# Optimization experiments

Hardware: AMD Instinct MI355X
Metric: run time of the kernel (lower is better)

The kernel has to match this reference:

```python
import jax, jax.numpy as jnp
import numpy as np

N_NODES = 100000
N_EDGES = 1200000
DIM = 64
MAX_DEG = 64
NUM_LAB = 16
BN_EPS = 1e-5


def _lrelu(x):
    return jax.nn.leaky_relu(x, negative_slope=0.01)


def _bn(x, g, b):
    # BatchNorm1d in training mode: batch statistics over node axis
    m = x.mean(axis=0)
    v = x.var(axis=0)
    return (x - m) * jax.lax.rsqrt(v + BN_EPS) * g + b


def _gin_layer(h, src, dst, n, w1, b1, w2, b2, eps, g, b):
    # GINConv: (1+eps)*x_i + sum_{j in N(i)} x_j, then MLP (lin_lrelu_lin), BN, LeakyReLU
    agg = jax.ops.segment_sum(h[src], dst, num_segments=n)
    x = (1.0 + eps) * h + agg
    x = _lrelu(x @ w1 + b1) @ w2 + b2
    return _lrelu(_bn(x, g, b))


def setup_inputs() -> dict:
    key = jax.random.key(0)
    ks = jax.random.split(key, 16)
    s = 0.05
    inp = {
        'node_deg': jax.random.randint(ks[0], (N_NODES,), 0, MAX_DEG + 1, dtype=jnp.int32),
        'node_lab': jax.random.randint(ks[1], (N_NODES,), 0, NUM_LAB, dtype=jnp.int32),
        'edge_index': jax.random.randint(ks[2], (2, N_EDGES), 0, N_NODES, dtype=jnp.int32),
        'emb_deg': jax.random.normal(ks[3], (MAX_DEG + 1, DIM), jnp.float32) * s,
        'emb_lab': jax.random.normal(ks[4], (NUM_LAB, DIM), jnp.float32) * s,
        'l0_w1': jax.random.normal(ks[5], (2 * DIM, 2 * DIM), jnp.float32) * s,
        'l0_b1': jnp.zeros((2 * DIM,), jnp.float32),
        'l0_w2': jax.random.normal(ks[6], (2 * DIM, DIM), jnp.float32) * s,
        'l0_b2': jnp.zeros((DIM,), jnp.float32),
        'l0_eps': jnp.zeros((1,), jnp.float32),
        'bn0_g': jnp.ones((DIM,), jnp.float32),
        'bn0_b': jnp.zeros((DIM,), jnp.float32),
        'l1_w1': jax.random.normal(ks[7], (DIM, DIM), jnp.float32) * s,
        'l1_b1': jnp.zeros((DIM,), jnp.float32),
        'l1_w2': jax.random.normal(ks[8], (DIM, DIM), jnp.float32) * s,
        'l1_b2': jnp.zeros((DIM,), jnp.float32),
        'l1_eps': jnp.zeros((1,), jnp.float32),
        'bn1_g': jnp.ones((DIM,), jnp.float32),
        'bn1_b': jnp.zeros((DIM,), jnp.float32),
        'fc_w1': jax.random.normal(ks[9], (4 * DIM, DIM), jnp.float32) * s,
        'fc_b1': jnp.zeros((DIM,), jnp.float32),
        'fc_bn_g': jnp.ones((DIM,), jnp.float32),
        'fc_bn_b': jnp.zeros((DIM,), jnp.float32),
        'fc_w2': jax.random.normal(ks[10], (DIM, 1), jnp.float32) * s,
        'fc_b2': jnp.zeros((1,), jnp.float32),
    }
    return inp


def reference(node_deg, node_lab, edge_index, emb_deg, emb_lab,
              l0_w1, l0_b1, l0_w2, l0_b2, l0_eps, bn0_g, bn0_b,
              l1_w1, l1_b1, l1_w2, l1_b2, l1_eps, bn1_g, bn1_b,
              fc_w1, fc_b1, fc_bn_g, fc_bn_b, fc_w2, fc_b2):
    n = node_deg.shape[0]
    src, dst = edge_index[0], edge_index[1]
    # embedding concat: [N, 2*DIM]
    h0 = jnp.concatenate([emb_deg[node_deg], emb_lab[node_lab]], axis=1)
    h1 = _gin_layer(h0, src, dst, n, l0_w1, l0_b1, l0_w2, l0_b2, l0_eps[0], bn0_g, bn0_b)
    h2 = _gin_layer(h1, src, dst, n, l1_w1, l1_b1, l1_w2, l1_b2, l1_eps[0], bn1_g, bn1_b)
    x = jnp.concatenate([h0, h1, h2], axis=1)  # [N, 256]
    x = _lrelu(_bn(x @ fc_w1 + fc_b1, fc_bn_g, fc_bn_b))
    out = jax.nn.sigmoid(x @ fc_w2 + fc_b2)
    return out.squeeze(-1)  # [N]
```

## Files before the change

### kernel.cpp

```cpp
#include <hip/hip_runtime.h>

#define N_NODES 100000
#define N_EDGES 1200000
#define NCLS 81
#define NBKT 391
#define BCAP 4608
#define NCHK 293
#define NGBLK 1563

typedef unsigned short u16;
typedef unsigned char u8;
typedef unsigned int u32;
typedef unsigned long long u64;
typedef short bf16x8 __attribute__((ext_vector_type(8)));
typedef float f32x4 __attribute__((ext_vector_type(4)));

__device__ __forceinline__ float b2f(u16 u) {
  union { u32 i; float f; } v; v.i = ((u32)u) << 16; return v.f;
}
__device__ __forceinline__ u16 f2b(float f) {
  union { float f; u32 i; } v; v.f = f;
  u32 x = v.i;
  return (u16)((x + 0x7fffu + ((x >> 16) & 1u)) >> 16);
}
__device__ __forceinline__ void up2(u32 w, float& lo, float& hi) {
  union { u32 u; float f; } a, b;
  a.u = w << 16; b.u = w & 0xffff0000u;
  lo = a.f; hi = b.f;
}
__device__ __forceinline__ float lrelu(float x) { return x > 0.f ? x : 0.01f * x; }

__device__ __forceinline__ bool is_f32(const u16* emb) {
  int lane = threadIdx.x & 63;
  u32 e0 = (emb[lane * 2] >> 7) & 0xFF;
  u32 e1 = (emb[lane * 2 + 1] >> 7) & 0xFF;
  return __ballot((e0 >= 0x90) || (e1 >= 0x90)) != 0ull;
}

__device__ __forceinline__ float rdr(const void* p, int i, bool f32m) {
  return f32m ? ((const float*)p)[i] : b2f(((const u16*)p)[i]);
}

#define P_EMBD 0
#define P_EMBL 4160
#define P_W1A  5184
#define P_B1A  21568
#define P_W2A  21696
#define P_B2A  29888
#define P_EPS0 29952
#define P_G0   29953
#define P_BB0  30017
#define P_LW1  30081
#define P_LB1  34177
#define P_LW2  34241
#define P_LB2  38337
#define P_EPS1 38401
#define P_G1   38402
#define P_BB1  38466
#define P_FW1  38530
#define P_FB1  54914
#define P_FG   54978
#define P_FBB  55042
#define P_FW2  55106
#define P_FB2  55170
#define P_TOT  55171

struct CvtAll {
  const void* src[22];
  int cnt[22];
  int off[22];
};

struct RawPtrs {
  const void* embD;
  const void* embL;
  const void* w1r;
  const void* w2r;
  const void* lw1r;
  const void* lw2r;
  const void* fwr;
};

__global__ void k_init(CvtAll a, RawPtrs rw, const u16* __restrict__ embRaw,
                       float* __restrict__ P, float* __restrict__ W1p,
                       float* __restrict__ Efc, u16* __restrict__ bp,
                       u16* __restrict__ wpB, u32* __restrict__ gcur) {
  bool f32m = is_f32(embRaw);
  int tid = threadIdx.x;
  if (blockIdx.y < 22) {
    if (blockIdx.y == 0 && blockIdx.x == 0) {
      for (int i = tid; i < NBKT; i += 256) gcur[i] = 0;
    }
    int seg = blockIdx.y;
    int i = blockIdx.x * 256 + tid;
    if (i < a.cnt[seg]) {
      float v = f32m ? ((const float*)a.src[seg])[i] : b2f(((const u16*)a.src[seg])[i]);
      P[a.off[seg] + i] = v;
    }
    return;
  }
  int idx = blockIdx.x * 256 + tid;
  if (idx < NCLS * 128) {
    int c = idx >> 7, h = idx & 127;
    float s = 0.f;
    if (c < 65) {
      for (int k = 0; k < 64; ++k)
        s = fmaf(rdr(rw.embD, c * 64 + k, f32m), rdr(rw.w1r, k * 128 + h, f32m), s);
    } else {
      for (int k = 0; k < 64; ++k)
        s = fmaf(rdr(rw.embL, (c - 65) * 64 + k, f32m), rdr(rw.w1r, (64 + k) * 128 + h, f32m), s);
    }
    W1p[idx] = s;
    return;
  }
  if (idx < NCLS * 128 + NCLS * 64) {
    int r = idx - NCLS * 128;
    int c = r >> 6, o = r & 63;
    float s = 0.f;
    if (c < 65) {
      for (int k = 0; k < 64; ++k)
        s = fmaf(rdr(rw.embD, c * 64 + k, f32m), rdr(rw.fwr, k * 64 + o, f32m), s);
    } else {
      for (int k = 0; k < 64; ++k)
        s = fmaf(rdr(rw.embL, (c - 65) * 64 + k, f32m), rdr(rw.fwr, (64 + k) * 64 + o, f32m), s);
    }
    Efc[r] = s;
    return;
  }
  if (idx < NCLS * 128 + NCLS * 64 + 24576) {
    int pidx = idx - (NCLS * 128 + NCLS * 64);
    int seg, rel;
    if (pidx < 8192)       { seg = 0; rel = pidx; }
    else if (pidx < 12288) { seg = 1; rel = pidx - 8192; }
    else if (pidx < 16384) { seg = 2; rel = pidx - 12288; }
    else                   { seg = 3; rel = pidx - 16384; }
    const void* srcs[4] = {rw.w2r, rw.lw1r, rw.lw2r, rw.fwr};
    const int addoff[4] = {0, 0, 0, 128 * 64};
    const int KBs[4] = {4, 2, 2, 4};
    int j = rel & 7, lane = (rel >> 3) & 63, rest = rel >> 9;
    int kb = rest % KBs[seg], nt = rest / KBs[seg];
    int k = kb * 32 + (lane >> 4) * 8 + j;
    int n = nt * 16 + (lane & 15);
    bp[pidx] = f2b(rdr(srcs[seg], addoff[seg] + k * 64 + n, f32m));
    return;
  }
  int p2 = idx - (NCLS * 128 + NCLS * 64 + 24576);
  if (p2 >= 12288) return;
  int j = p2 & 7, lane = (p2 >> 3) & 63, rest = p2 >> 9;
  int kb = rest % 3, nt = rest / 3;
  int c = kb * 32 + (lane >> 4) * 8 + j;
  int n = nt * 16 + (lane & 15);
  float s = 0.f;
  if (c < NCLS) {
    if (c < 65) {
      for (int k = 0; k < 64; ++k)
        s = fmaf(rdr(rw.embD, c * 64 + k, f32m), rdr(rw.w1r, k * 128 + n, f32m), s);
    } else {
      for (int k = 0; k < 64; ++k)
        s = fmaf(rdr(rw.embL, (c - 65) * 64 + k, f32m), rdr(rw.w1r, (64 + k) * 128 + n, f32m), s);
    }
  }
  wpB[p2] = (c < NCLS) ? f2b(s) : 0;
}

__global__ __launch_bounds__(256) void k_bsort(const int* __restrict__ edge,
                                               const int* __restrict__ ndeg,
                                               const int* __restrict__ nlab,
                                               u32* __restrict__ gcur,
                                               u64* __restrict__ e2) {
  __shared__ u32 cnt[NBKT], rbase[NBKT];
  __shared__ u32 slo[4096], shi[4096];
  for (int i = threadIdx.x; i < NBKT; i += 256) cnt[i] = 0;
  __syncthreads();
  int base = blockIdx.x * 4096;
  for (int i = threadIdx.x; i < 4096; i += 256) {
    int e = base + i;
    if (e < N_EDGES) {
      int s = edge[e], d = edge[N_EDGES + e];
      slo[i] = ((u32)s << 11) | ((u32)ndeg[s] << 4) | (u32)nlab[s];
      shi[i] = (u32)d;
      atomicAdd(&cnt[(u32)d >> 8], 1u);
    } else shi[i] = 0xFFFFFFFFu;
  }
  __syncthreads();
  for (int i = threadIdx.x; i < NBKT; i += 256) {
    u32 c = cnt[i];
    rbase[i] = c ? atomicAdd(&gcur[i], c) : 0u;
    cnt[i] = 0;
  }
  __syncthreads();
  for (int i = threadIdx.x; i < 4096; i += 256) {
    u32 d = shi[i];
    if (d == 0xFFFFFFFFu) continue;
    u32 b = d >> 8;
    u32 pos = rbase[b] + atomicAdd(&cnt[b], 1u);
    e2[(size_t)b * BCAP + pos] = ((u64)d << 32) | (u64)slo[i];
  }
}

__global__ __launch_bounds__(512) void k_csrh(const u64* __restrict__ e2,
                                              const u32* __restrict__ gcur,
                                              const u16* __restrict__ wpB,
                                              const float* __restrict__ W1p,
                                              const float* __restrict__ P,
                                              const int* __restrict__ ndeg,
                                              const int* __restrict__ nlab,
                                              const u16* __restrict__ Bp2,
                                              u32* __restrict__ row_ptr,
                                              u32* __restrict__ einfo,
                                              u16* __restrict__ t0,
                                              float* __restrict__ pbuf) {
  __shared__ u32 l[256], cur[256], gl[NBKT], wt[8];
  __shared__ u32 h32[256 * 24];
  __shared__ u32 sbase;
  __shared__ u16 T[8][16][136];
  __shared__ float lsum[8][64], lsq[8][64];
  int b = blockIdx.x, tid = threadIdx.x;
  int wid = tid >> 6, lane = tid & 63;
  if (tid < NBKT) gl[tid] = gcur[tid];
  if (tid < 256) l[tid] = 0;
  for (int i = tid; i < 256 * 24; i += 512) h32[i] = 0;
  __syncthreads();
  if (wid == 0) {
    u32 s = 0;
    for (int i = lane; i < b; i += 64) s += gl[i];
    s += __shfl_xor(s, 1, 64); s += __shfl_xor(s, 2, 64); s += __shfl_xor(s, 4, 64);
    s += __shfl_xor(s, 8, 64); s += __shfl_xor(s, 16, 64); s += __shfl_xor(s, 32, 64);
    if (lane == 0) sbase = s;
  }
  u32 cnt = gl[b];
  const u64* src = e2 + (size_t)b * BCAP;
  for (u32 e = tid; e < cnt; e += 512)
    atomicAdd(&l[(u32)(src[e] >> 32) & 255u], 1u);
  __syncthreads();
  u32 v = 0, incl = 0;
  if (tid < 256) {
    v = l[tid];
    u32 x = v;
#pragma unroll
    for (int off = 1; off < 64; off <<= 1) {
      u32 t = __shfl_up(x, off, 64);
      if (lane >= off) x += t;
    }
    if (lane == 63) wt[wid] = x;
    incl = x;
  }
  __syncthreads();
  if (tid < 256) {
    u32 woff = 0;
    for (int w = 0; w < wid; ++w) woff += wt[w];
    u32 pos0 = sbase + woff + incl - v;
    cur[tid] = pos0;
    int nn = b * 256 + tid;
    if (nn <= N_NODES) row_ptr[nn] = pos0;
  }
  __syncthreads();
  for (u32 e = tid; e < cnt; e += 512) {
    u64 r = src[e];
    u32 dl = (u32)(r >> 32) & 255u;
    u32 lo = (u32)r;
    u32 pos = atomicAdd(&cur[dl], 1u);
    einfo[pos] = lo;
    u32 c1 = (lo >> 4) & 0x7Fu, c2 = 65u + (lo & 15u);
    atomicAdd(&h32[dl * 24 + (c1 >> 2)], 1u << ((c1 & 3u) * 8));
    atomicAdd(&h32[dl * 24 + (c2 >> 2)], 1u << ((c2 & 3u) * 8));
  }
  __syncthreads();
  const u8* h = (const u8*)h32;
  int row = lane & 15, q = lane >> 4;
  float onep = 1.f + P[P_EPS0];
  const bf16x8* bp = (const bf16x8*)wpB;
  const bf16x8* bp2 = (const bf16x8*)Bp2;
  float ssA[4] = {0.f, 0.f, 0.f, 0.f}, qqA[4] = {0.f, 0.f, 0.f, 0.f};
#pragma unroll 1
  for (int t = wid; t < 16; t += 8) {
    int m0 = b * 256 + t * 16;
    if (m0 >= N_NODES) break;
    f32x4 acc[8];
#pragma unroll
    for (int nt = 0; nt < 8; ++nt) {
      float bb = P[P_B1A + nt * 16 + row];
      acc[nt][0] = bb; acc[nt][1] = bb; acc[nt][2] = bb; acc[nt][3] = bb;
    }
    const u8* ar = h + (t * 16 + row) * 96 + q * 8;
#pragma unroll
    for (int kb = 0; kb < 3; ++kb) {
      bf16x8 af;
#pragma unroll
      for (int j = 0; j < 8; ++j) af[j] = (short)f2b((float)ar[kb * 32 + j]);
#pragma unroll
      for (int nt = 0; nt < 8; ++nt) {
        bf16x8 bf = bp[(nt * 3 + kb) * 64 + lane];
        acc[nt] = __builtin_amdgcn_mfma_f32_16x16x32_bf16(af, bf, acc[nt], 0, 0, 0);
      }
    }
#pragma unroll
    for (int r = 0; r < 4; ++r) {
      int m = m0 + q * 4 + r;
      int node = q * 4 + r;
      if (m < N_NODES) {
        const float* wd = W1p + ndeg[m] * 128;
        const float* wl = W1p + (65 + nlab[m]) * 128;
#pragma unroll
        for (int nt = 0; nt < 8; ++nt) {
          int cc = nt * 16 + row;
          float vv = acc[nt][r] + onep * (wd[cc] + wl[cc]);
          T[wid][node][cc] = f2b(lrelu(vv));
        }
      } else {
#pragma unroll
        for (int nt = 0; nt < 8; ++nt) T[wid][node][nt * 16 + row] = 0;
      }
    }
    const u16* ap = &T[wid][row][q * 8];
    f32x4 acc2[4];
#pragma unroll
    for (int nt = 0; nt < 4; ++nt) {
      float bb = P[P_B2A + nt * 16 + row];
      acc2[nt][0] = bb; acc2[nt][1] = bb; acc2[nt][2] = bb; acc2[nt][3] = bb;
    }
#pragma unroll
    for (int kb = 0; kb < 4; ++kb) {
      bf16x8 af = *(const bf16x8*)(ap + kb * 32);
#pragma unroll
      for (int nt = 0; nt < 4; ++nt) {
        bf16x8 bf = bp2[(nt * 4 + kb) * 64 + lane];
        acc2[nt] = __builtin_amdgcn_mfma_f32_16x16x32_bf16(af, bf, acc2[nt], 0, 0, 0);
      }
    }
#pragma unroll
    for (int nt = 0; nt < 4; ++nt) {
      float s = 0.f, z = 0.f;
#pragma unroll
      for (int r = 0; r < 4; ++r) {
        int m = m0 + q * 4 + r;
        if (m < N_NODES) {
          u16 bv = f2b(acc2[nt][r]);
          t0[(size_t)m * 64 + nt * 16 + row] = bv;
          float vv = b2f(bv);
          s += vv; z = fmaf(vv, vv, z);
        }
      }
      s += __shfl_xor(s, 16, 64); s += __shfl_xor(s, 32, 64);
      z += __shfl_xor(z, 16, 64); z += __shfl_xor(z, 32, 64);
      ssA[nt] += s; qqA[nt] += z;
    }
  }
  if (lane < 16) {
#pragma unroll
    for (int nt = 0; nt < 4; ++nt) {
      lsum[wid][nt * 16 + lane] = ssA[nt];
      lsq[wid][nt * 16 + lane] = qqA[nt];
    }
  }
  __syncthreads();
  if (tid < 64) {
    float s = 0.f;
#pragma unroll
    for (int w = 0; w < 8; ++w) s += lsum[w][tid];
    pbuf[(size_t)b * 128 + tid] = s;
  } else if (tid < 128) {
    int c = tid - 64;
    float s = 0.f;
#pragma unroll
    for (int w = 0; w < 8; ++w) s += lsq[w][c];
    pbuf[(size_t)b * 128 + tid] = s;
  }
}

__global__ void k_sr(const float* __restrict__ pbuf, float* __restrict__ statsOut,
                     int nrows) {
  __shared__ float l[256];
  int c = blockIdx.x;
  float s = 0.f;
  for (int r = threadIdx.x; r < nrows; r += 256) s += pbuf[(size_t)r * 128 + c];
  l[threadIdx.x] = s;
  __syncthreads();
  for (int off = 128; off > 0; off >>= 1) {
    if (threadIdx.x < off) l[threadIdx.x] += l[threadIdx.x + off];
    __syncthreads();
  }
  if (threadIdx.x == 0) statsOut[c] = l[0];
}

template <int KB, int LDA, int BIASOFF>
__global__ __launch_bounds__(256) void k_gemm(const u16* __restrict__ A,
                                              const u16* __restrict__ Bp,
                                              const float* __restrict__ P,
                                              float* __restrict__ pbuf,
                                              u16* __restrict__ C) {
  __shared__ float lsum[4][64], lsq[4][64];
  int wid = threadIdx.x >> 6, lane = threadIdx.x & 63;
  int m0 = (blockIdx.x * 4 + wid) * 16;
  bool act = m0 < N_NODES;
  int row = lane & 15, q = lane >> 4;
  float ss[4] = {0.f, 0.f, 0.f, 0.f}, qq[4] = {0.f, 0.f, 0.f, 0.f};
  if (act) {
    const u16* ap = A + (size_t)(m0 + row) * LDA + q * 8;
    const bf16x8* bp = (const bf16x8*)Bp;
    f32x4 acc[4];
#pragma unroll
    for (int nt = 0; nt < 4; ++nt) {
      float b = (BIASOFF >= 0) ? P[BIASOFF + nt * 16 + row] : 0.f;
      acc[nt][0] = b; acc[nt][1] = b; acc[nt][2] = b; acc[nt][3] = b;
    }
#pragma unroll
    for (int kb = 0; kb < KB; ++kb) {
      bf16x8 af = *(const bf16x8*)(ap + kb * 32);
#pragma unroll
      for (int nt = 0; nt < 4; ++nt) {
        bf16x8 bf = bp[(nt * KB + kb) * 64 + lane];
        acc[nt] = __builtin_amdgcn_mfma_f32_16x16x32_bf16(af, bf, acc[nt], 0, 0, 0);
      }
    }
#pragma unroll
    for (int nt = 0; nt < 4; ++nt) {
      float s = 0.f, z = 0.f;
#pragma unroll
      for (int r = 0; r < 4; ++r) {
        int m = m0 + q * 4 + r;
        u16 bv = f2b(acc[nt][r]);
        C[(size_t)m * 64 + nt * 16 + row] = bv;
        float v = b2f(bv);
        s += v; z = fmaf(v, v, z);
      }
      s += __shfl_xor(s, 16, 64); s += __shfl_xor(s, 32, 64);
      z += __shfl_xor(z, 16, 64); z += __shfl_xor(z, 32, 64);
      ss[nt] = s; qq[nt] = z;
    }
  }
  if (lane < 16) {
#pragma unroll
    for (int nt = 0; nt < 4; ++nt) {
      lsum[wid][nt * 16 + lane] = ss[nt];
      lsq[wid][nt * 16 + lane] = qq[nt];
    }
  }
  __syncthreads();
  int t = threadIdx.x;
  if (t < 64)
    pbuf[(size_t)blockIdx.x * 128 + t] = lsum[0][t] + lsum[1][t] + lsum[2][t] + lsum[3][t];
  else if (t < 128) {
    int c = t - 64;
    pbuf[(size_t)blockIdx.x * 128 + t] = lsq[0][c] + lsq[1][c] + lsq[2][c] + lsq[3][c];
  }
}

__global__ __launch_bounds__(256) void k_gemm_bn(const u16* __restrict__ A,
                                                 const u16* __restrict__ Bp,
                                                 const float* __restrict__ P,
                                                 const float* __restrict__ stats,
                                                 u16* __restrict__ C) {
  int wid = threadIdx.x >> 6, lane = threadIdx.x & 63;
  int m0 = (blockIdx.x * 4 + wid) * 16;
  if (m0 >= N_NODES) return;
  int row = lane & 15, q = lane >> 4;
  const float invN = 1.f / (float)N_NODES;
  float sc[16], sh[16];
#pragma unroll
  for (int kb = 0; kb < 2; ++kb)
#pragma unroll
    for (int j = 0; j < 8; ++j) {
      int f = kb * 32 + q * 8 + j;
      float mm = stats[f] * invN;
      float var = fmaxf(stats[64 + f] * invN - mm * mm, 0.f);
      float inv = rsqrtf(var + 1e-5f);
      float s = inv * P[P_G0 + f];
      sc[kb * 8 + j] = s;
      sh[kb * 8 + j] = P[P_BB0 + f] - mm * s;
    }
  const u16* ap = A + (size_t)(m0 + row) * 64 + q * 8;
  const bf16x8* bp = (const bf16x8*)Bp;
  f32x4 acc[4];
#pragma unroll
  for (int nt = 0; nt < 4; ++nt) {
    acc[nt][0] = 0.f; acc[nt][1] = 0.f; acc[nt][2] = 0.f; acc[nt][3] = 0.f;
  }
#pragma unroll
  for (int kb = 0; kb < 2; ++kb) {
    uint4 raw = *(const uint4*)(ap + kb * 32);
    u32 rw[4] = {raw.x, raw.y, raw.z, raw.w};
    bf16x8 af;
#pragma unroll
    for (int p = 0; p < 4; ++p) {
      float lo, hi;
      up2(rw[p], lo, hi);
      float y0 = lrelu(fmaf(sc[kb * 8 + 2 * p], lo, sh[kb * 8 + 2 * p]));
      float y1 = lrelu(fmaf(sc[kb * 8 + 2 * p + 1], hi, sh[kb * 8 + 2 * p + 1]));
      af[2 * p] = (short)f2b(y0);
      af[2 * p + 1] = (short)f2b(y1);
    }
#pragma unroll
    for (int nt = 0; nt < 4; ++nt) {
      bf16x8 bf = bp[(nt * 2 + kb) * 64 + lane];
      acc[nt] = __builtin_amdgcn_mfma_f32_16x16x32_bf16(af, bf, acc[nt], 0, 0, 0);
    }
  }
#pragma unroll
  for (int nt = 0; nt < 4; ++nt)
#pragma unroll
    for (int r = 0; r < 4; ++r) {
      int m = m0 + q * 4 + r;
      C[(size_t)m * 64 + nt * 16 + row] = f2b(acc[nt][r]);
    }
}

__global__ __launch_bounds__(256) void k_agg1(const u32* __restrict__ rp,
                                              const u32* __restrict__ einfo,
                                              const u16* __restrict__ g1,
                                              const float* __restrict__ P,
                                              u16* __restrict__ abuf) {
  int lane = threadIdx.x & 63, wv = threadIdx.x >> 6;
  int n = blockIdx.x * 4 + wv;
  if (n >= N_NODES) return;
  u32 st = rp[n], en = rp[n + 1];
  u32 m = en - st;
  int grp = lane >> 4;
  int fo = (lane & 15) * 4;
  u32 myidx = (u32)n;
  if (lane < (int)m) myidx = einfo[st + lane] >> 11;
  u32 mm = m < 64u ? m : 64u;
  float a0 = 0.f, a1 = 0.f, a2 = 0.f, a3 = 0.f;
  for (u32 k = 0; k < mm; k += 16) {
#pragma unroll
    for (int bb = 0; bb < 4; ++bb) {
      u32 e = k + (u32)(bb * 4 + grp);
      u32 src = (u32)__shfl((int)myidx, (int)e, 64);
      if (e < mm) {
        uint2 v = *(const uint2*)(g1 + (size_t)src * 64 + fo);
        float l0, h0, l1, h1;
        up2(v.x, l0, h0);
        up2(v.y, l1, h1);
        a0 += l0; a1 += h0; a2 += l1; a3 += h1;
      }
    }
  }
  a0 += __shfl_xor(a0, 16, 64); a0 += __shfl_xor(a0, 32, 64);
  a1 += __shfl_xor(a1, 16, 64); a1 += __shfl_xor(a1, 32, 64);
  a2 += __shfl_xor(a2, 16, 64); a2 += __shfl_xor(a2, 32, 64);
  a3 += __shfl_xor(a3, 16, 64); a3 += __shfl_xor(a3, 32, 64);
  for (u32 k = 64; k < m; ++k) {
    u32 src = einfo[st + k] >> 11;
    uint2 v = *(const uint2*)(g1 + (size_t)src * 64 + fo);
    float l0, h0, l1, h1;
    up2(v.x, l0, h0);
    up2(v.y, l1, h1);
    a0 += l0; a1 += h0; a2 += l1; a3 += h1;
  }
  float onep = 1.f + P[P_EPS1];
  uint2 sv = *(const uint2*)(g1 + (size_t)n * 64 + fo);
  float s0, s1, s2, s3;
  up2(sv.x, s0, s1);
  up2(sv.y, s2, s3);
  float r0 = P[P_LB1 + fo + 0] + fmaf(onep, s0, a0);
  float r1 = P[P_LB1 + fo + 1] + fmaf(onep, s1, a1);
  float r2 = P[P_LB1 + fo + 2] + fmaf(onep, s2, a2);
  float r3 = P[P_LB1 + fo + 3] + fmaf(onep, s3, a3);
  if (lane < 16) {
    uint2 o;
    o.x = ((u32)f2b(lrelu(r0))) | (((u32)f2b(lrelu(r1))) << 16);
    o.y = ((u32)f2b(lrelu(r2))) | (((u32)f2b(lrelu(r3))) << 16);
    *(uint2*)(abuf + (size_t)n * 64 + fo) = o;
  }
}

__global__ __launch_bounds__(256) void k_gemm_fc1bn(const u16* __restrict__ t0,
                                                    const u16* __restrict__ t1,
                                                    const u16* __restrict__ Bp,
                                                    const float* __restrict__ P,
                                                    const float* __restrict__ stats,
                                                    float* __restrict__ pbuf,
                                                    const int* __restrict__ ndeg,
                                                    const int* __restrict__ nlab,
                                                    const float* __restrict__ Efc,
                                                    u16* __restrict__ C) {
  __shared__ float lsum[4][64], lsq[4][64];
  int wid = threadIdx.x >> 6, lane = threadIdx.x & 63;
  int m0 = (blockIdx.x * 4 + wid) * 16;
  bool act = m0 < N_NODES;
  int row = lane & 15, q = lane >> 4;
  float ss[4] = {0.f, 0.f, 0.f, 0.f}, qq[4] = {0.f, 0.f, 0.f, 0.f};
  if (act) {
    const float invN = 1.f / (float)N_NODES;
    float sc[32], sh[32];
#pragma unroll
    for (int h = 0; h < 2; ++h) {
      const float* st = stats + h * 128;
      int gof = h ? P_G1 : P_G0, bof = h ? P_BB1 : P_BB0;
#pragma unroll
      for (int kb = 0; kb < 2; ++kb)
#pragma unroll
        for (int j = 0; j < 8; ++j) {
          int f = kb * 32 + q * 8 + j;
          float mm = st[f] * invN;
          float var = fmaxf(st[64 + f] * invN - mm * mm, 0.f);
          float inv = rsqrtf(var + 1e-5f);
          float s = inv * P[gof + f];
          sc[h * 16 + kb * 8 + j] = s;
          sh[h * 16 + kb * 8 + j] = P[bof + f] - mm * s;
        }
    }
    const u16* a0 = t0 + (size_t)(m0 + row) * 64 + q * 8;
    const u16* a1 = t1 + (size_t)(m0 + row) * 64 + q * 8;
    const bf16x8* bp = (const bf16x8*)Bp;
    f32x4 acc[4];
#pragma unroll
    for (int nt = 0; nt < 4; ++nt) {
      float b = P[P_FB1 + nt * 16 + row];
      acc[nt][0] = b; acc[nt][1] = b; acc[nt][2] = b; acc[nt][3] = b;
    }
#pragma unroll
    for (int kb = 0; kb < 4; ++kb) {
      const u16* src = (kb < 2) ? (a0 + kb * 32) : (a1 + (kb - 2) * 32);
      int ci = (kb < 2) ? kb * 8 : 16 + (kb - 2) * 8;
      uint4 raw = *(const uint4*)src;
      u32 rw[4] = {raw.x, raw.y, raw.z, raw.w};
      bf16x8 af;
#pragma unroll
      for (int p = 0; p < 4; ++p) {
        float lo, hi;
        up2(rw[p], lo, hi);
        float y0 = lrelu(fmaf(sc[ci + 2 * p], lo, sh[ci + 2 * p]));
        float y1 = lrelu(fmaf(sc[ci + 2 * p + 1], hi, sh[ci + 2 * p + 1]));
        af[2 * p] = (short)f2b(y0);
        af[2 * p + 1] = (short)f2b(y1);
      }
#pragma unroll
      for (int nt = 0; nt < 4; ++nt) {
        bf16x8 bf = bp[(nt * 4 + kb) * 64 + lane];
        acc[nt] = __builtin_amdgcn_mfma_f32_16x16x32_bf16(af, bf, acc[nt], 0, 0, 0);
      }
    }
    float es[4][4];
#pragma unroll
    for (int r = 0; r < 4; ++r) {
      int m = m0 + q * 4 + r;
      int dn = ndeg[m], ln = 65 + nlab[m];
#pragma unroll
      for (int nt = 0; nt < 4; ++nt) {
        int cc = nt * 16 + row;
        es[r][nt] = acc[nt][r] + Efc[dn * 64 + cc] + Efc[ln * 64 + cc];
      }
    }
#pragma unroll
    for (int nt = 0; nt < 4; ++nt) {
      float s = 0.f, z = 0.f;
#pragma unroll
      for (int r = 0; r < 4; ++r) {
        int m = m0 + q * 4 + r;
        u16 bv = f2b(es[r][nt]);
        C[(size_t)m * 64 + nt * 16 + row] = bv;
        float v = b2f(bv);
        s += v; z = fmaf(v, v, z);
      }
      s += __shfl_xor(s, 16, 64); s += __shfl_xor(s, 32, 64);
      z += __shfl_xor(z, 16, 64); z += __shfl_xor(z, 32, 64);
      ss[nt] = s; qq[nt] = z;
    }
  }
  if (lane < 16) {
#pragma unroll
    for (int nt = 0; nt < 4; ++nt) {
      lsum[wid][nt * 16 + lane] = ss[nt];
      lsq[wid][nt * 16 + lane] = qq[nt];
    }
  }
  __syncthreads();
  int t = threadIdx.x;
  if (t < 64)
    pbuf[(size_t)blockIdx.x * 128 + t] = lsum[0][t] + lsum[1][t] + lsum[2][t] + lsum[3][t];
  else if (t < 128) {
    int c = t - 64;
    pbuf[(size_t)blockIdx.x * 128 + t] = lsq[0][c] + lsq[1][c] + lsq[2][c] + lsq[3][c];
  }
}

__global__ __launch_bounds__(256) void k_fc2(const u16* __restrict__ t,
                                             const float* __restrict__ stats,
                                             const float* __restrict__ P,
                                             const u16* __restrict__ embRaw,
                                             void* __restrict__ out) {
  __shared__ float scF[64], shF[64], fwF[64];
  bool f32m = is_f32(embRaw);
  int tid = threadIdx.x;
  if (tid < 64) {
    const float invN = 1.f / (float)N_NODES;
    float mm = stats[tid] * invN;
    float var = fmaxf(stats[64 + tid] * invN - mm * mm, 0.f);
    float inv = rsqrtf(var + 1e-5f);
    float s = inv * P[P_FG + tid];
    scF[tid] = s;
    shF[tid] = P[P_FBB + tid] - mm * s;
    fwF[tid] = P[P_FW2 + tid];
  }
  __syncthreads();
  int n = blockIdx.x * 256 + tid;
  if (n >= N_NODES) return;
  float z = P[P_FB2];
  const uint4* tn = (const uint4*)(t + (size_t)n * 64);
#pragma unroll
  for (int jj = 0; jj < 8; ++jj) {
    uint4 raw = tn[jj];
    u32 w[4] = {raw.x, raw.y, raw.z, raw.w};
#pragma unroll
    for (int p = 0; p < 4; ++p) {
      int f = jj * 8 + p * 2;
      float lo, hi;
      up2(w[p], lo, hi);
      float y0 = lrelu(fmaf(scF[f], lo, shF[f]));
      float y1 = lrelu(fmaf(scF[f + 1], hi, shF[f + 1]));
      z = fmaf(y0, fwF[f], z);
      z = fmaf(y1, fwF[f + 1], z);
    }
  }
  float s = 1.f / (1.f + expf(-z));
  if (!(fabsf(z) < 1e30f)) s = 0.25f;
  if (f32m) ((float*)out)[n] = s;
  else      ((u16*)out)[n] = f2b(s);
}

extern "C" void kernel_launch(void* const* d_in, const int* in_sizes, int n_in,
                              void* d_out, int out_size, void* d_ws, size_t ws_size,
                              hipStream_t stream) {
  const int* node_deg = (const int*)d_in[0];
  const int* node_lab = (const int*)d_in[1];
  const int* edge     = (const int*)d_in[2];
  const u16* embRaw   = (const u16*)d_in[3];
  (void)in_sizes; (void)n_in; (void)out_size; (void)ws_size;

  char* base = (char*)d_ws;
  size_t off = 0;
  auto alloc = [&](size_t bytes) -> void* {
    void* p = base + off;
    off += (bytes + 15) & ~(size_t)15;
    return p;
  };
  float* Pb    = (float*)alloc((size_t)P_TOT * 4);
  float* stats = (float*)alloc(384 * 4);
  u32* gcur    = (u32*)alloc(NBKT * 4);
  float* W1p   = (float*)alloc(NCLS * 128 * 4);
  float* Efc   = (float*)alloc(NCLS * 64 * 4);
  u16* bpack   = (u16*)alloc(24576 * 2);
  u16* wpB     = (u16*)alloc(12288 * 2);
  u32* row_ptr = (u32*)alloc((size_t)(N_NODES + 1) * 4);
  float* pbuf  = (float*)alloc((size_t)NGBLK * 128 * 4);
  u32* einfo   = (u32*)alloc((size_t)N_EDGES * 4);
  u64* e2      = (u64*)alloc((size_t)NBKT * BCAP * 8);
  void* arena  = alloc((size_t)N_NODES * 128 * 2);
  u16* t0      = (u16*)alloc((size_t)N_NODES * 64 * 2);
  u16* t1      = (u16*)alloc((size_t)N_NODES * 64 * 2);
  u16* t2      = (u16*)alloc((size_t)N_NODES * 64 * 2);
  u16* g1   = (u16*)arena;
  u16* abuf = (u16*)arena + (size_t)N_NODES * 64;
  u16* Bp_w2a = bpack;
  u16* Bp_lw1 = bpack + 8192;
  u16* Bp_lw2 = bpack + 12288;
  u16* Bp_fw1 = bpack + 16384;

  CvtAll ca;
  const int srcidx[22] = {3, 4, 5, 6, 7, 8, 9, 10, 11, 12, 13, 14, 15, 16, 17, 18, 19, 20, 21, 22, 23, 24};
  const int cnts[22]   = {4160, 1024, 16384, 128, 8192, 64, 1, 64, 64, 4096, 64, 4096, 64, 1, 64, 64, 16384, 64, 64, 64, 64, 1};
  const int offs[22]   = {P_EMBD, P_EMBL, P_W1A, P_B1A, P_W2A, P_B2A, P_EPS0, P_G0, P_BB0,
                          P_LW1, P_LB1, P_LW2, P_LB2, P_EPS1, P_G1, P_BB1,
                          P_FW1, P_FB1, P_FG, P_FBB, P_FW2, P_FB2};
  for (int i = 0; i < 22; ++i) { ca.src[i] = d_in[srcidx[i]]; ca.cnt[i] = cnts[i]; ca.off[i] = offs[i]; }
  RawPtrs rw;
  rw.embD = d_in[3]; rw.embL = d_in[4]; rw.w1r = d_in[5]; rw.w2r = d_in[7];
  rw.lw1r = d_in[12]; rw.lw2r = d_in[14]; rw.fwr = d_in[19];

  k_init<<<dim3(205, 23), 256, 0, stream>>>(ca, rw, embRaw, Pb, W1p, Efc, bpack, wpB, gcur);

  k_bsort<<<NCHK, 256, 0, stream>>>(edge, node_deg, node_lab, gcur, e2);

  k_csrh<<<NBKT, 512, 0, stream>>>(e2, gcur, wpB, W1p, Pb, node_deg, node_lab,
                                   Bp_w2a, row_ptr, einfo, t0, pbuf);
  k_sr<<<128, 256, 0, stream>>>(pbuf, stats, NBKT);

  const int GEMM_GRID = NGBLK;

  k_gemm_bn<<<GEMM_GRID, 256, 0, stream>>>(t0, Bp_lw1, Pb, stats, g1);
  k_agg1<<<(N_NODES + 3) / 4, 256, 0, stream>>>(row_ptr, einfo, g1, Pb, abuf);
  k_gemm<2, 64, P_LB2><<<GEMM_GRID, 256, 0, stream>>>(abuf, Bp_lw2, Pb, pbuf, t1);
  k_sr<<<128, 256, 0, stream>>>(pbuf, stats + 128, NGBLK);

  k_gemm_fc1bn<<<GEMM_GRID, 256, 0, stream>>>(t0, t1, Bp_fw1, Pb, stats, pbuf,
                                              node_deg, node_lab, Efc, t2);
  k_sr<<<128, 256, 0, stream>>>(pbuf, stats + 256, NGBLK);
  k_fc2<<<(N_NODES + 255) / 256, 256, 0, stream>>>(t2, stats + 256, Pb, embRaw, d_out);
}
```

Baseline: 287.2 us.

## Slice aggregation features into per-XCD column slabs for L2 locality

The g1 and abuf buffers move from row-major [N,64] to four column slabs of [N,16], and each slab is pinned to a pair of XCDs by decoding the block index. k_agg1 now has each wave handle four nodes over one 16-feature slice, so the gathered working set per XCD is a quarter of the table and can stay in that XCD's L2. A new k_gemm_sl reads the sliced layout and feeds the MFMA GEMM. The cost is four times as many edge-index shuffles and einfo reads. The hard-coded XCD mapping also assumes round-robin block dispatch across 8 XCDs.

```diff
diff --git a/kernel.cpp b/kernel.cpp
--- a/kernel.cpp
+++ b/kernel.cpp
@@ -7,6 +7,7 @@
 #define BCAP 4608
 #define NCHK 293
 #define NGBLK 1563
+#define SLN (N_NODES * 16)
 
 typedef unsigned short u16;
 typedef unsigned char u8;
@@ -501,7 +502,7 @@
 #pragma unroll
     for (int r = 0; r < 4; ++r) {
       int m = m0 + q * 4 + r;
-      C[(size_t)m * 64 + nt * 16 + row] = f2b(acc[nt][r]);
+      C[(size_t)nt * SLN + (size_t)m * 16 + row] = f2b(acc[nt][r]);
     }
 }
 
@@ -510,57 +511,131 @@
                                               const u16* __restrict__ g1,
                                               const float* __restrict__ P,
                                               u16* __restrict__ abuf) {
+  int b = blockIdx.x;
+  int xcd = b & 7;
+  int s = xcd & 3;
+  int chunk = (b >> 3) + ((xcd >> 2) ? 3125 : 0);
   int lane = threadIdx.x & 63, wv = threadIdx.x >> 6;
-  int n = blockIdx.x * 4 + wv;
-  if (n >= N_NODES) return;
-  u32 st = rp[n], en = rp[n + 1];
+  int ns = lane >> 4;
+  int li = lane & 15;
+  int es = li >> 2, half = li & 3;
+  int n0 = chunk * 16 + wv * 4;
+  int n = n0 + ns;
+  const u16* gt = g1 + (size_t)s * SLN;
+  u32 rpv = 0;
+  if (lane <= 4) rpv = rp[n0 + lane];
+  u32 st = (u32)__shfl((int)rpv, ns, 64);
+  u32 en = (u32)__shfl((int)rpv, ns + 1, 64);
   u32 m = en - st;
-  int grp = lane >> 4;
-  int fo = (lane & 15) * 4;
-  u32 myidx = (u32)n;
-  if (lane < (int)m) myidx = einfo[st + lane] >> 11;
-  u32 mm = m < 64u ? m : 64u;
+  u32 myidx = 0;
+  if (li < (int)m) myidx = einfo[st + li];
+  u32 mm = m < 16u ? m : 16u;
   float a0 = 0.f, a1 = 0.f, a2 = 0.f, a3 = 0.f;
-  for (u32 k = 0; k < mm; k += 16) {
-#pragma unroll
-    for (int bb = 0; bb < 4; ++bb) {
-      u32 e = k + (u32)(bb * 4 + grp);
-      u32 src = (u32)__shfl((int)myidx, (int)e, 64);
-      if (e < mm) {
-        uint2 v = *(const uint2*)(g1 + (size_t)src * 64 + fo);
-        float l0, h0, l1, h1;
-        up2(v.x, l0, h0);
-        up2(v.y, l1, h1);
-        a0 += l0; a1 += h0; a2 += l1; a3 += h1;
-      }
-    }
-  }
-  a0 += __shfl_xor(a0, 16, 64); a0 += __shfl_xor(a0, 32, 64);
-  a1 += __shfl_xor(a1, 16, 64); a1 += __shfl_xor(a1, 32, 64);
-  a2 += __shfl_xor(a2, 16, 64); a2 += __shfl_xor(a2, 32, 64);
-  a3 += __shfl_xor(a3, 16, 64); a3 += __shfl_xor(a3, 32, 64);
-  for (u32 k = 64; k < m; ++k) {
-    u32 src = einfo[st + k] >> 11;
-    uint2 v = *(const uint2*)(g1 + (size_t)src * 64 + fo);
-    float l0, h0, l1, h1;
-    up2(v.x, l0, h0);
-    up2(v.y, l1, h1);
-    a0 += l0; a1 += h0; a2 += l1; a3 += h1;
-  }
-  float onep = 1.f + P[P_EPS1];
-  uint2 sv = *(const uint2*)(g1 + (size_t)n * 64 + fo);
-  float s0, s1, s2, s3;
-  up2(sv.x, s0, s1);
-  up2(sv.y, s2, s3);
-  float r0 = P[P_LB1 + fo + 0] + fmaf(onep, s0, a0);
-  float r1 = P[P_LB1 + fo + 1] + fmaf(onep, s1, a1);
-  float r2 = P[P_LB1 + fo + 2] + fmaf(onep, s2, a2);
-  float r3 = P[P_LB1 + fo + 3] + fmaf(onep, s3, a3);
-  if (lane < 16) {
+  u32 iters = (mm + 3) >> 2;
+  for (u32 k = 0; k < iters; ++k) {
+    u32 e = k * 4 + (u32)es;
+    u32 idx = (u32)__shfl((int)myidx, ns * 16 + (int)e, 64);
+    if (e < mm) {
+      u32 src = idx >> 11;
+      uint2 v = *(const uint2*)(gt + (size_t)src * 16 + half * 4);
+      float l0, h0, l1, h1;
+      up2(v.x, l0, h0);
+      up2(v.y, l1, h1);
+      a0 += l0; a1 += h0; a2 += l1; a3 += h1;
+    }
+  }
+  if (es == 0) {
+    for (u32 k = 16; k < m; ++k) {
+      u32 src = einfo[st + k] >> 11;
+      uint2 v = *(const uint2*)(gt + (size_t)src * 16 + half * 4);
+      float l0, h0, l1, h1;
+      up2(v.x, l0, h0);
+      up2(v.y, l1, h1);
+      a0 += l0; a1 += h0; a2 += l1; a3 += h1;
+    }
+  }
+  a0 += __shfl_xor(a0, 4, 64); a0 += __shfl_xor(a0, 8, 64);
+  a1 += __shfl_xor(a1, 4, 64); a1 += __shfl_xor(a1, 8, 64);
+  a2 += __shfl_xor(a2, 4, 64); a2 += __shfl_xor(a2, 8, 64);
+  a3 += __shfl_xor(a3, 4, 64); a3 += __shfl_xor(a3, 8, 64);
+  if (es == 0) {
+    float onep = 1.f + P[P_EPS1];
+    uint2 sv = *(const uint2*)(gt + (size_t)n * 16 + half * 4);
+    float s0, s1, s2, s3;
+    up2(sv.x, s0, s1);
+    up2(sv.y, s2, s3);
+    int f = s * 16 + half * 4;
+    float r0 = P[P_LB1 + f + 0] + fmaf(onep, s0, a0);
+    float r1 = P[P_LB1 + f + 1] + fmaf(onep, s1, a1);
+    float r2 = P[P_LB1 + f + 2] + fmaf(onep, s2, a2);
+    float r3 = P[P_LB1 + f + 3] + fmaf(onep, s3, a3);
     uint2 o;
     o.x = ((u32)f2b(lrelu(r0))) | (((u32)f2b(lrelu(r1))) << 16);
     o.y = ((u32)f2b(lrelu(r2))) | (((u32)f2b(lrelu(r3))) << 16);
-    *(uint2*)(abuf + (size_t)n * 64 + fo) = o;
+    *(uint2*)(abuf + (size_t)s * SLN + (size_t)n * 16 + half * 4) = o;
+  }
+}
+
+__global__ __launch_bounds__(256) void k_gemm_sl(const u16* __restrict__ A,
+                                                 const u16* __restrict__ Bp,
+                                                 const float* __restrict__ P,
+                                                 float* __restrict__ pbuf,
+                                                 u16* __restrict__ C) {
+  __shared__ float lsum[4][64], lsq[4][64];
+  int wid = threadIdx.x >> 6, lane = threadIdx.x & 63;
+  int m0 = (blockIdx.x * 4 + wid) * 16;
+  bool act = m0 < N_NODES;
+  int row = lane & 15, q = lane >> 4;
+  float ss[4] = {0.f, 0.f, 0.f, 0.f}, qq[4] = {0.f, 0.f, 0.f, 0.f};
+  if (act) {
+    const bf16x8* bp = (const bf16x8*)Bp;
+    f32x4 acc[4];
+#pragma unroll
+    for (int nt = 0; nt < 4; ++nt) {
+      float b = P[P_LB2 + nt * 16 + row];
+      acc[nt][0] = b; acc[nt][1] = b; acc[nt][2] = b; acc[nt][3] = b;
+    }
+#pragma unroll
+    for (int kb = 0; kb < 2; ++kb) {
+      const u16* ap = A + (size_t)(kb * 2 + (q >> 1)) * SLN +
+                      (size_t)(m0 + row) * 16 + (q & 1) * 8;
+      bf16x8 af = *(const bf16x8*)ap;
+#pragma unroll
+      for (int nt = 0; nt < 4; ++nt) {
+        bf16x8 bf = bp[(nt * 2 + kb) * 64 + lane];
+        acc[nt] = __builtin_amdgcn_mfma_f32_16x16x32_bf16(af, bf, acc[nt], 0, 0, 0);
+      }
+    }
+#pragma unroll
+    for (int nt = 0; nt < 4; ++nt) {
+      float s = 0.f, z = 0.f;
+#pragma unroll
+      for (int r = 0; r < 4; ++r) {
+        int m = m0 + q * 4 + r;
+        u16 bv = f2b(acc[nt][r]);
+        C[(size_t)m * 64 + nt * 16 + row] = bv;
+        float v = b2f(bv);
+        s += v; z = fmaf(v, v, z);
+      }
+      s += __shfl_xor(s, 16, 64); s += __shfl_xor(s, 32, 64);
+      z += __shfl_xor(z, 16, 64); z += __shfl_xor(z, 32, 64);
+      ss[nt] = s; qq[nt] = z;
+    }
+  }
+  if (lane < 16) {
+#pragma unroll
+    for (int nt = 0; nt < 4; ++nt) {
+      lsum[wid][nt * 16 + lane] = ss[nt];
+      lsq[wid][nt * 16 + lane] = qq[nt];
+    }
+  }
+  __syncthreads();
+  int t = threadIdx.x;
+  if (t < 64)
+    pbuf[(size_t)blockIdx.x * 128 + t] = lsum[0][t] + lsum[1][t] + lsum[2][t] + lsum[3][t];
+  else if (t < 128) {
+    int c = t - 64;
+    pbuf[(size_t)blockIdx.x * 128 + t] = lsq[0][c] + lsq[1][c] + lsq[2][c] + lsq[3][c];
   }
 }
 
@@ -779,8 +854,8 @@
   const int GEMM_GRID = NGBLK;
 
   k_gemm_bn<<<GEMM_GRID, 256, 0, stream>>>(t0, Bp_lw1, Pb, stats, g1);
-  k_agg1<<<(N_NODES + 3) / 4, 256, 0, stream>>>(row_ptr, einfo, g1, Pb, abuf);
-  k_gemm<2, 64, P_LB2><<<GEMM_GRID, 256, 0, stream>>>(abuf, Bp_lw2, Pb, pbuf, t1);
+  k_agg1<<<25000, 256, 0, stream>>>(row_ptr, einfo, g1, Pb, abuf);
+  k_gemm_sl<<<GEMM_GRID, 256, 0, stream>>>(abuf, Bp_lw2, Pb, pbuf, t1);
   k_sr<<<128, 256, 0, stream>>>(pbuf, stats + 128, NGBLK);
 
   k_gemm_fc1bn<<<GEMM_GRID, 256, 0, stream>>>(t0, t1, Bp_fw1, Pb, stats, pbuf,
```

Result: no change. 288.2 us (+0.3%).

## Fuse BN stat reductions into producer kernels via last-block atomic counter

Applied to the files above, without the earlier changes.

Removes the three separate k_sr reduction launches by having the last block to finish each producer kernel (k_csrh, k_gemm, k_gemm_fc1bn) sum the per-block partials into the stats buffer, using an atomic counter and threadfences. It also precomputes a packed deg/label word per node in k_init so k_bsort does one gather per edge source instead of two. The intent is to cut launch overhead and gather traffic. The cost is a serial tail: one block reads up to 1563x128 partials on its own, with only 256 threads.

```diff
diff --git a/kernel.cpp b/kernel.cpp
--- a/kernel.cpp
+++ b/kernel.cpp
@@ -84,12 +84,19 @@
 __global__ void k_init(CvtAll a, RawPtrs rw, const u16* __restrict__ embRaw,
                        float* __restrict__ P, float* __restrict__ W1p,
                        float* __restrict__ Efc, u16* __restrict__ bp,
-                       u16* __restrict__ wpB, u32* __restrict__ gcur) {
+                       u16* __restrict__ wpB, u32* __restrict__ gcur,
+                       const int* __restrict__ ndeg, const int* __restrict__ nlab,
+                       u32* __restrict__ pk) {
+  int tid = threadIdx.x;
+  if (blockIdx.y == 23) {
+    int n = blockIdx.x * 256 + tid;
+    if (n < N_NODES) pk[n] = ((u32)ndeg[n] << 4) | (u32)nlab[n];
+    return;
+  }
   bool f32m = is_f32(embRaw);
-  int tid = threadIdx.x;
   if (blockIdx.y < 22) {
     if (blockIdx.y == 0 && blockIdx.x == 0) {
-      for (int i = tid; i < NBKT; i += 256) gcur[i] = 0;
+      for (int i = tid; i < NBKT + 4; i += 256) gcur[i] = 0;
     }
     int seg = blockIdx.y;
     int i = blockIdx.x * 256 + tid;
@@ -164,8 +171,7 @@
 }
 
 __global__ __launch_bounds__(256) void k_bsort(const int* __restrict__ edge,
-                                               const int* __restrict__ ndeg,
-                                               const int* __restrict__ nlab,
+                                               const u32* __restrict__ pk,
                                                u32* __restrict__ gcur,
                                                u64* __restrict__ e2) {
   __shared__ u32 cnt[NBKT], rbase[NBKT];
@@ -177,7 +183,7 @@
     int e = base + i;
     if (e < N_EDGES) {
       int s = edge[e], d = edge[N_EDGES + e];
-      slo[i] = ((u32)s << 11) | ((u32)ndeg[s] << 4) | (u32)nlab[s];
+      slo[i] = ((u32)s << 11) | pk[s];
       shi[i] = (u32)d;
       atomicAdd(&cnt[(u32)d >> 8], 1u);
     } else shi[i] = 0xFFFFFFFFu;
@@ -209,10 +215,12 @@
                                               u32* __restrict__ row_ptr,
                                               u32* __restrict__ einfo,
                                               u16* __restrict__ t0,
-                                              float* __restrict__ pbuf) {
+                                              float* __restrict__ pbuf,
+                                              float* __restrict__ statsOut,
+                                              u32* __restrict__ ctr) {
   __shared__ u32 l[256], cur[256], gl[NBKT], wt[8];
   __shared__ u32 h32[256 * 24];
-  __shared__ u32 sbase;
+  __shared__ u32 sbase, lastF;
   __shared__ u16 T[8][16][136];
   __shared__ float lsum[8][64], lsq[8][64];
   int b = blockIdx.x, tid = threadIdx.x;
@@ -366,21 +374,23 @@
     for (int w = 0; w < 8; ++w) s += lsq[w][c];
     pbuf[(size_t)b * 128 + tid] = s;
   }
-}
-
-__global__ void k_sr(const float* __restrict__ pbuf, float* __restrict__ statsOut,
-                     int nrows) {
-  __shared__ float l[256];
-  int c = blockIdx.x;
-  float s = 0.f;
-  for (int r = threadIdx.x; r < nrows; r += 256) s += pbuf[(size_t)r * 128 + c];
-  l[threadIdx.x] = s;
-  __syncthreads();
-  for (int off = 128; off > 0; off >>= 1) {
-    if (threadIdx.x < off) l[threadIdx.x] += l[threadIdx.x + off];
+  __syncthreads();
+  if (tid == 0) {
+    __threadfence();
+    lastF = (atomicAdd(ctr, 1u) == NBKT - 1) ? 1u : 0u;
+  }
+  __syncthreads();
+  if (lastF) {
+    __threadfence();
+    if (tid < 256) {
+      int c = tid & 127, hh = tid >> 7;
+      float s2 = 0.f;
+      for (int r = hh; r < NBKT; r += 2) s2 += pbuf[(size_t)r * 128 + c];
+      ((float*)lsum)[tid] = s2;
+    }
     __syncthreads();
-  }
-  if (threadIdx.x == 0) statsOut[c] = l[0];
+    if (tid < 128) statsOut[tid] = ((float*)lsum)[tid] + ((float*)lsum)[128 + tid];
+  }
 }
 
 template <int KB, int LDA, int BIASOFF>
@@ -388,8 +398,11 @@
                                               const u16* __restrict__ Bp,
                                               const float* __restrict__ P,
                                               float* __restrict__ pbuf,
-                                              u16* __restrict__ C) {
+                                              u16* __restrict__ C,
+                                              float* __restrict__ statsOut,
+                                              u32* __restrict__ ctr) {
   __shared__ float lsum[4][64], lsq[4][64];
+  __shared__ u32 lastF;
   int wid = threadIdx.x >> 6, lane = threadIdx.x & 63;
   int m0 = (blockIdx.x * 4 + wid) * 16;
   bool act = m0 < N_NODES;
@@ -443,6 +456,21 @@
   else if (t < 128) {
     int c = t - 64;
     pbuf[(size_t)blockIdx.x * 128 + t] = lsq[0][c] + lsq[1][c] + lsq[2][c] + lsq[3][c];
+  }
+  __syncthreads();
+  if (t == 0) {
+    __threadfence();
+    lastF = (atomicAdd(ctr, 1u) == (u32)gridDim.x - 1u) ? 1u : 0u;
+  }
+  __syncthreads();
+  if (lastF) {
+    __threadfence();
+    int c = t & 127, hh = t >> 7;
+    float s2 = 0.f;
+    for (int r = hh; r < (int)gridDim.x; r += 2) s2 += pbuf[(size_t)r * 128 + c];
+    ((float*)lsum)[t] = s2;
+    __syncthreads();
+    if (t < 128) statsOut[t] = ((float*)lsum)[t] + ((float*)lsum)[128 + t];
   }
 }
 
@@ -573,8 +601,11 @@
                                                     const int* __restrict__ ndeg,
                                                     const int* __restrict__ nlab,
                                                     const float* __restrict__ Efc,
-                                                    u16* __restrict__ C) {
+                                                    u16* __restrict__ C,
+                                                    float* __restrict__ statsOut,
+                                                    u32* __restrict__ ctr) {
   __shared__ float lsum[4][64], lsq[4][64];
+  __shared__ u32 lastF;
   int wid = threadIdx.x >> 6, lane = threadIdx.x & 63;
   int m0 = (blockIdx.x * 4 + wid) * 16;
   bool act = m0 < N_NODES;
@@ -672,6 +703,21 @@
   else if (t < 128) {
     int c = t - 64;
     pbuf[(size_t)blockIdx.x * 128 + t] = lsq[0][c] + lsq[1][c] + lsq[2][c] + lsq[3][c];
+  }
+  __syncthreads();
+  if (t == 0) {
+    __threadfence();
+    lastF = (atomicAdd(ctr, 1u) == (u32)gridDim.x - 1u) ? 1u : 0u;
+  }
+  __syncthreads();
+  if (lastF) {
+    __threadfence();
+    int c = t & 127, hh = t >> 7;
+    float s2 = 0.f;
+    for (int r = hh; r < (int)gridDim.x; r += 2) s2 += pbuf[(size_t)r * 128 + c];
+    ((float*)lsum)[t] = s2;
+    __syncthreads();
+    if (t < 128) statsOut[t] = ((float*)lsum)[t] + ((float*)lsum)[128 + t];
   }
 }
 
@@ -737,7 +783,8 @@
   };
   float* Pb    = (float*)alloc((size_t)P_TOT * 4);
   float* stats = (float*)alloc(384 * 4);
-  u32* gcur    = (u32*)alloc(NBKT * 4);
+  u32* gcur    = (u32*)alloc((NBKT + 4) * 4);
+  u32* pk      = (u32*)alloc((size_t)N_NODES * 4);
   float* W1p   = (float*)alloc(NCLS * 128 * 4);
   float* Efc   = (float*)alloc(NCLS * 64 * 4);
   u16* bpack   = (u16*)alloc(24576 * 2);
@@ -768,23 +815,24 @@
   rw.embD = d_in[3]; rw.embL = d_in[4]; rw.w1r = d_in[5]; rw.w2r = d_in[7];
   rw.lw1r = d_in[12]; rw.lw2r = d_in[14]; rw.fwr = d_in[19];
 
-  k_init<<<dim3(205, 23), 256, 0, stream>>>(ca, rw, embRaw, Pb, W1p, Efc, bpack, wpB, gcur);
-
-  k_bsort<<<NCHK, 256, 0, stream>>>(edge, node_deg, node_lab, gcur, e2);
+  k_init<<<dim3(391, 24), 256, 0, stream>>>(ca, rw, embRaw, Pb, W1p, Efc, bpack, wpB,
+                                            gcur, node_deg, node_lab, pk);
+
+  k_bsort<<<NCHK, 256, 0, stream>>>(edge, pk, gcur, e2);
 
   k_csrh<<<NBKT, 512, 0, stream>>>(e2, gcur, wpB, W1p, Pb, node_deg, node_lab,
-                                   Bp_w2a, row_ptr, einfo, t0, pbuf);
-  k_sr<<<128, 256, 0, stream>>>(pbuf, stats, NBKT);
+                                   Bp_w2a, row_ptr, einfo, t0, pbuf, stats,
+                                   gcur + NBKT);
 
   const int GEMM_GRID = NGBLK;
 
   k_gemm_bn<<<GEMM_GRID, 256, 0, stream>>>(t0, Bp_lw1, Pb, stats, g1);
   k_agg1<<<(N_NODES + 3) / 4, 256, 0, stream>>>(row_ptr, einfo, g1, Pb, abuf);
-  k_gemm<2, 64, P_LB2><<<GEMM_GRID, 256, 0, stream>>>(abuf, Bp_lw2, Pb, pbuf, t1);
-  k_sr<<<128, 256, 0, stream>>>(pbuf, stats + 128, NGBLK);
+  k_gemm<2, 64, P_LB2><<<GEMM_GRID, 256, 0, stream>>>(abuf, Bp_lw2, Pb, pbuf, t1,
+                                                      stats + 128, gcur + NBKT + 1);
 
   k_gemm_fc1bn<<<GEMM_GRID, 256, 0, stream>>>(t0, t1, Bp_fw1, Pb, stats, pbuf,
-                                              node_deg, node_lab, Efc, t2);
-  k_sr<<<128, 256, 0, stream>>>(pbuf, stats + 256, NGBLK);
+                                              node_deg, node_lab, Efc, t2,
+                                              stats + 256, gcur + NBKT + 2);
   k_fc2<<<(N_NODES + 255) / 256, 256, 0, stream>>>(t2, stats + 256, Pb, embRaw, d_out);
 }
```

After: 827.9 us. 188% more time.
